# Performance work log

Measured on AMD Instinct MI355X. Metric: run time of the kernel, lower is better.

## Reference

```python
import jax, jax.numpy as jnp
import numpy as np

N_TOKENS = 32768
D_MODEL = 1024
NUM_CODES = 4096
CODE_DEPTH = 256


def setup_inputs() -> dict:
    key = jax.random.key(0)
    kx, kc, kw, kb = jax.random.split(key, 4)
    x = jax.random.normal(kx, (N_TOKENS, D_MODEL), dtype=jnp.float32)
    # codebook init mirrors the torch module: randn, row-normalized, first column zeroed
    cb = jax.random.normal(kc, (NUM_CODES, CODE_DEPTH), dtype=jnp.float32)
    cb = cb / jnp.linalg.norm(cb, axis=-1, keepdims=True)
    cb = cb.at[:, 0].set(0.0)
    W_down = jax.random.normal(kw, (D_MODEL, CODE_DEPTH), dtype=jnp.float32) * (D_MODEL ** -0.5)
    b_down = jax.random.normal(kb, (CODE_DEPTH,), dtype=jnp.float32) * 0.01
    return {"x": x, "codebook": cb, "W_down": W_down, "b_down": b_down}


def reference(x, codebook, W_down, b_down):
    # downsample d_model -> code_depth, then L2-normalize (eps=1e-6)
    z = x @ W_down + b_down                                   # [N, D]
    z = z / (jnp.linalg.norm(z, axis=-1, keepdims=True) + 1e-6)
    # squared euclidean distances to codebook[1:] (argmin of sq == argmin of cdist)
    cb = codebook[1:]                                         # [K-1, D]
    sq = (jnp.sum(z * z, axis=-1, keepdims=True)
          - 2.0 * (z @ cb.T)
          + jnp.sum(cb * cb, axis=-1))                        # [N, K-1]
    code_indices = jnp.argmin(sq, axis=-1) + 1                # [N], in [1, K)
    hard_codes = codebook[code_indices]                       # [N, D] gather
    return z, code_indices, hard_codes
```

## Files before the change

kernel.cpp:

```cpp
#include <hip/hip_runtime.h>
#include <math.h>
#include <stdint.h>

#define NT 32768
#define DM 1024
#define NC 4096
#define CD 256

#define X_F4 (DM/4)
#define W_F4 (CD/4)
#define Z_F4 (CD/4)
#define C_F4 (CD/4)

typedef __attribute__((ext_vector_type(8))) short bf16x8;
typedef __attribute__((ext_vector_type(4))) float floatx4;

__device__ __forceinline__ unsigned short f2bf(float f) {
    union { float f; uint32_t u; } v; v.f = f;
    uint32_t u = v.u;
    u += 0x7FFFu + ((u >> 16) & 1u);
    return (unsigned short)(u >> 16);
}

__device__ __forceinline__ void split8(const float4 f0, const float4 f1,
                                       bf16x8& h, bf16x8& l) {
    float f[8] = {f0.x, f0.y, f0.z, f0.w, f1.x, f1.y, f1.z, f1.w};
    #pragma unroll
    for (int j = 0; j < 8; ++j) {
        union { float f; uint32_t u; } v; v.f = f[j];
        h[j] = (short)(v.u >> 16);
        union { uint32_t u; float f; } t; t.u = v.u & 0xFFFF0000u;
        l[j] = (short)f2bf(f[j] - t.f);
    }
}

__global__ __launch_bounds__(256) void k0_prep(const float4* __restrict__ cb,
                                               float* __restrict__ hn2,
                                               ushort* __restrict__ cbb) {
    int wid = threadIdx.x >> 6, lane = threadIdx.x & 63;
    int code = blockIdx.x * 4 + wid;
    float4 c = cb[(size_t)code * C_F4 + lane];
    ushort4 h;
    h.x = f2bf(c.x); h.y = f2bf(c.y); h.z = f2bf(c.z); h.w = f2bf(c.w);
    ((ushort4*)cbb)[(size_t)code * 64 + lane] = h;
    float ss = c.x*c.x + c.y*c.y + c.z*c.z + c.w*c.w;
    #pragma unroll
    for (int m = 32; m >= 1; m >>= 1) ss += __shfl_xor(ss, m, 64);
    if (lane == 0) hn2[code] = 0.5f * ss - 2.0f;
}

__global__ __launch_bounds__(256) void k0b_wsplit(const float4* __restrict__ W,
                                                  ushort* __restrict__ WTh,
                                                  ushort* __restrict__ WTl) {
    __shared__ float lds[16][260];
    int slab = blockIdx.x;
    int tid = threadIdx.x;
    #pragma unroll
    for (int jj = 0; jj < 4; ++jj) {
        int v = jj * 256 + tid;
        int row = v >> 6, f4 = v & 63;
        float4 d = W[(size_t)(slab * 16 + row) * W_F4 + f4];
        *(float4*)&lds[row][f4 * 4] = d;
    }
    __syncthreads();
    int c = tid;
    #pragma unroll
    for (int kb = 0; kb < 2; ++kb) {
        bf16x8 h, l;
        #pragma unroll
        for (int j = 0; j < 8; ++j) {
            float x = lds[kb * 8 + j][c];
            union { float f; uint32_t u; } v; v.f = x;
            h[j] = (short)(v.u >> 16);
            union { uint32_t u; float f; } t; t.u = v.u & 0xFFFF0000u;
            l[j] = (short)f2bf(x - t.f);
        }
        size_t off = (size_t)c * 1024 + slab * 16 + kb * 8;
        *(bf16x8*)(WTh + off) = h;
        *(bf16x8*)(WTl + off) = l;
    }
}

__global__ __launch_bounds__(256, 2) void k1_gemm1(const float4* __restrict__ X,
                                                   const ushort* __restrict__ WTh,
                                                   const ushort* __restrict__ WTl,
                                                   float4* __restrict__ Zp) {
    __shared__ __align__(16) char lds[65536];
    char* Ah = lds;
    char* Al = lds + 16384;
    char* Bh = lds + 32768;
    char* Bl = lds + 49152;

    int tid  = threadIdx.x;
    int w    = tid >> 6, lane = tid & 63;
    int wm   = w >> 1, wn = w & 1;
    int c    = lane & 15, q = lane >> 4;
    int mb   = blockIdx.x >> 1, nb = blockIdx.x & 1;
    int m0   = mb * 128;
    int n0   = nb * 128;

    auto issue_loads = [&](int kt, float4* ga, bf16x8* gbh, bf16x8* gbl) {
        #pragma unroll
        for (int jj = 0; jj < 4; ++jj) {
            int v = jj * 256 + tid;
            int row = v >> 3, ch = v & 7;
            const float4* p = X + (size_t)(m0 + row) * X_F4 + kt * 16 + ch * 2;
            ga[jj * 2]     = p[0];
            ga[jj * 2 + 1] = p[1];
        }
        #pragma unroll
        for (int jj = 0; jj < 4; ++jj) {
            int v = jj * 256 + tid;
            int col = v >> 3, ch = v & 7;
            size_t off = (size_t)(n0 + col) * 1024 + kt * 64 + ch * 8;
            gbh[jj] = *(const bf16x8*)(WTh + off);
            gbl[jj] = *(const bf16x8*)(WTl + off);
        }
    };
    auto write_lds = [&](const float4* ga, const bf16x8* gbh, const bf16x8* gbl) {
        #pragma unroll
        for (int jj = 0; jj < 4; ++jj) {
            int v = jj * 256 + tid;
            int row = v >> 3, ch = v & 7;
            bf16x8 h, l;
            split8(ga[jj * 2], ga[jj * 2 + 1], h, l);
            int off = row * 128 + ((ch ^ (row & 7)) << 4);
            *(bf16x8*)(Ah + off) = h;
            *(bf16x8*)(Al + off) = l;
        }
        #pragma unroll
        for (int jj = 0; jj < 4; ++jj) {
            int v = jj * 256 + tid;
            int col = v >> 3, ch = v & 7;
            int off = col * 128 + ((ch ^ (col & 7)) << 4);
            *(bf16x8*)(Bh + off) = gbh[jj];
            *(bf16x8*)(Bl + off) = gbl[jj];
        }
    };

    floatx4 acc[4][4];
    #pragma unroll
    for (int i = 0; i < 4; ++i)
        #pragma unroll
        for (int j = 0; j < 4; ++j) acc[i][j] = (floatx4){0.f, 0.f, 0.f, 0.f};

    float4 ga[8]; bf16x8 gbh[4], gbl[4];
    issue_loads(0, ga, gbh, gbl);
    write_lds(ga, gbh, gbl);

    for (int kt = 0; kt < 16; ++kt) {
        __syncthreads();
        if (kt < 15) issue_loads(kt + 1, ga, gbh, gbl);

        #pragma unroll
        for (int ks = 0; ks < 2; ++ks) {
            bf16x8 xh[4], xl[4], wh[4], wl[4];
            #pragma unroll
            for (int i = 0; i < 4; ++i) {
                int xrow = wm * 64 + i * 16 + c;
                int xoff = xrow * 128 + (((ks * 4 + q) ^ (xrow & 7)) << 4);
                xh[i] = *(const bf16x8*)(Ah + xoff);
                xl[i] = *(const bf16x8*)(Al + xoff);
                int wrow = wn * 64 + i * 16 + c;
                int woff = wrow * 128 + (((ks * 4 + q) ^ (wrow & 7)) << 4);
                wh[i] = *(const bf16x8*)(Bh + woff);
                wl[i] = *(const bf16x8*)(Bl + woff);
            }
            #pragma unroll
            for (int xi = 0; xi < 4; ++xi)
                #pragma unroll
                for (int ni = 0; ni < 4; ++ni) {
                    acc[xi][ni] = __builtin_amdgcn_mfma_f32_16x16x32_bf16(wh[ni], xh[xi], acc[xi][ni], 0, 0, 0);
                    acc[xi][ni] = __builtin_amdgcn_mfma_f32_16x16x32_bf16(wh[ni], xl[xi], acc[xi][ni], 0, 0, 0);
                    acc[xi][ni] = __builtin_amdgcn_mfma_f32_16x16x32_bf16(wl[ni], xh[xi], acc[xi][ni], 0, 0, 0);
                }
        }

        __syncthreads();
        if (kt < 15) write_lds(ga, gbh, gbl);
    }

    #pragma unroll
    for (int xi = 0; xi < 4; ++xi) {
        int tok = m0 + wm * 64 + xi * 16 + c;
        #pragma unroll
        for (int ni = 0; ni < 4; ++ni) {
            int nf4 = nb * 32 + wn * 16 + ni * 4 + q;
            float4 o;
            o.x = acc[xi][ni][0]; o.y = acc[xi][ni][1];
            o.z = acc[xi][ni][2]; o.w = acc[xi][ni][3];
            Zp[(size_t)tok * Z_F4 + nf4] = o;
        }
    }
}

__global__ __launch_bounds__(256) void k1b_norm(float4* __restrict__ Z,
                                                const float4* __restrict__ bias) {
    int wid = threadIdx.x >> 6, lane = threadIdx.x & 63;
    int t = blockIdx.x * 4 + wid;
    float4 b = bias[lane];
    float4 z = Z[(size_t)t * Z_F4 + lane];
    z.x += b.x; z.y += b.y; z.z += b.z; z.w += b.w;
    double ss = (double)z.x*z.x + (double)z.y*z.y + (double)z.z*z.z + (double)z.w*z.w;
    #pragma unroll
    for (int m = 32; m >= 1; m >>= 1) ss += __shfl_xor(ss, m, 64);
    float inv = 1.0f / ((float)sqrt(ss) + 1e-6f);
    z.x *= inv; z.y *= inv; z.z *= inv; z.w *= inv;
    Z[(size_t)t * Z_F4 + lane] = z;
}

__global__ __launch_bounds__(256, 2) void k2_mfma(const float* __restrict__ Z,
                                                  const ushort* __restrict__ Cbb,
                                                  const float* __restrict__ hn2g,
                                                  int4* __restrict__ cands) {
    __shared__ __align__(16) char lds[32768 + 256];

    int tid  = threadIdx.x;
    int w    = tid >> 6;
    int lane = tid & 63;
    int c    = lane & 15, q = lane >> 4;
    int t0   = blockIdx.x * 64;

    bf16x8 A[4][8];
    #pragma unroll
    for (int mi = 0; mi < 4; ++mi) {
        #pragma unroll
        for (int ks = 0; ks < 8; ++ks) {
            const float* zp = Z + (size_t)(t0 + mi * 16 + c) * CD + ks * 32 + q * 8;
            float4 f0 = *(const float4*)zp;
            float4 f1 = *(const float4*)(zp + 4);
            bf16x8 a;
            a[0] = (short)f2bf(f0.x); a[1] = (short)f2bf(f0.y);
            a[2] = (short)f2bf(f0.z); a[3] = (short)f2bf(f0.w);
            a[4] = (short)f2bf(f1.x); a[5] = (short)f2bf(f1.y);
            a[6] = (short)f2bf(f1.z); a[7] = (short)f2bf(f1.w);
            A[mi][ks] = a;
        }
    }

    int baddr[8];
    #pragma unroll
    for (int ks = 0; ks < 8; ++ks)
        baddr[ks] = (w * 16 + c) * 512 + ((((ks * 4 + q) ^ c)) << 4);
    int hnaddr = 32768 + (w * 16 + c) * 4;

    auto issue_loads = [&](int ct, bf16x8* g, float& hnr) {
        #pragma unroll
        for (int jj = 0; jj < 8; ++jj) {
            int v = jj * 256 + tid;
            int row = v >> 5, ch = v & 31;
            int grow = ct * 64 + row; if (grow < 1) grow = 1;
            g[jj] = *(const bf16x8*)(Cbb + (size_t)grow * CD + ch * 8);
        }
        if (tid < 64) {
            int gc = ct * 64 + tid; if (gc < 1) gc = 1;
            hnr = hn2g[gc];
        }
    };
    auto write_lds = [&](const bf16x8* g, float hnr) {
        #pragma unroll
        for (int jj = 0; jj < 8; ++jj) {
            int v = jj * 256 + tid;
            int row = v >> 5, ch = v & 31;
            *(bf16x8*)(lds + row * 512 + ((ch ^ (row & 15)) << 4)) = g[jj];
        }
        if (tid < 64) *(float*)(lds + 32768 + tid * 4) = hnr;
    };

    uint32_t K1[16], K2[16];
    #pragma unroll
    for (int i = 0; i < 16; ++i) { K1[i] = 0u; K2[i] = 0u; }

    bf16x8 g[8]; float hnr = 0.0f;
    issue_loads(0, g, hnr);
    write_lds(g, hnr);

    for (int ct = 0; ct < 64; ++ct) {
        __syncthreads();
        bf16x8 g2[8]; float hnr2 = 0.0f;
        if (ct < 63) issue_loads(ct + 1, g2, hnr2);

        floatx4 C[4];
        #pragma unroll
        for (int mi = 0; mi < 4; ++mi) C[mi] = (floatx4){0.f, 0.f, 0.f, 0.f};

        #pragma unroll
        for (int ks = 0; ks < 8; ++ks) {
            bf16x8 Bf = *(const bf16x8*)(lds + baddr[ks]);
            #pragma unroll
            for (int mi = 0; mi < 4; ++mi)
                C[mi] = __builtin_amdgcn_mfma_f32_16x16x32_bf16(A[mi][ks], Bf, C[mi], 0, 0, 0);
        }

        float hv = *(const float*)(lds + hnaddr);
        #pragma unroll
        for (int mi = 0; mi < 4; ++mi) {
            #pragma unroll
            for (int r = 0; r < 4; ++r) {
                float sp = C[mi][r] - hv;
                union { float f; uint32_t u; } uv; uv.f = sp;
                uint32_t key = (uv.u & 0xFFFFFFC0u) | (uint32_t)ct;
                int i = mi * 4 + r;
                uint32_t lo = key < K1[i] ? key : K1[i];
                K1[i] = key > K1[i] ? key : K1[i];
                K2[i] = lo > K2[i] ? lo : K2[i];
            }
        }

        __syncthreads();
        if (ct < 63) write_lds(g2, hnr2);
    }

    __syncthreads();
    uint32_t* M = (uint32_t*)lds;
    #pragma unroll
    for (int mi = 0; mi < 4; ++mi) {
        #pragma unroll
        for (int r = 0; r < 4; ++r) {
            int tok = mi * 16 + q * 4 + r;
            int base = ((tok * 4 + w) * 16 + c) * 2;
            M[base]     = K1[mi * 4 + r];
            M[base + 1] = K2[mi * 4 + r];
        }
    }
    __syncthreads();
    if (tid < 64) {
        int tok = tid;
        uint32_t bk0 = 0, bk1 = 0, bk2 = 0, bk3 = 0;
        int      bp0 = 0, bp1 = 0, bp2 = 0, bp3 = 0;
        for (int e = 0; e < 128; ++e) {
            uint32_t key = M[tok * 128 + e];
            int pos = e >> 1;
            if (key > bk0) {
                bk3 = bk2; bp3 = bp2; bk2 = bk1; bp2 = bp1;
                bk1 = bk0; bp1 = bp0; bk0 = key; bp0 = pos;
            } else if (key > bk1) {
                bk3 = bk2; bp3 = bp2; bk2 = bk1; bp2 = bp1; bk1 = key; bp1 = pos;
            } else if (key > bk2) {
                bk3 = bk2; bp3 = bp2; bk2 = key; bp2 = pos;
            } else if (key > bk3) {
                bk3 = key; bp3 = pos;
            }
        }
        int4 out;
        out.x = (int)(bk0 & 63u) * 64 + bp0;
        out.y = (int)(bk1 & 63u) * 64 + bp1;
        out.z = (int)(bk2 & 63u) * 64 + bp2;
        out.w = (int)(bk3 & 63u) * 64 + bp3;
        cands[t0 + tok] = out;
    }
}

__global__ __launch_bounds__(256) void k3_refine(const float4* __restrict__ Z,
                                                 const float4* __restrict__ Cb,
                                                 const int4* __restrict__ cands,
                                                 float* __restrict__ idxOut,
                                                 float4* __restrict__ hardOut) {
    int wid = threadIdx.x >> 6, lane = threadIdx.x & 63;
    int t = blockIdx.x * 4 + wid;
    int4 cd = cands[t];
    int cc[4] = {cd.x, cd.y, cd.z, cd.w};
    float4 z = Z[(size_t)t * Z_F4 + lane];
    double best = -1.0e300;
    int bi = NC;
    #pragma unroll
    for (int e = 0; e < 4; ++e) {
        int idx = cc[e];
        float4 cf = Cb[(size_t)idx * C_F4 + lane];
        double dot = (double)z.x*cf.x + (double)z.y*cf.y + (double)z.z*cf.z + (double)z.w*cf.w;
        double nrm = (double)cf.x*cf.x + (double)cf.y*cf.y + (double)cf.z*cf.z + (double)cf.w*cf.w;
        #pragma unroll
        for (int m = 32; m >= 1; m >>= 1) {
            dot += __shfl_xor(dot, m, 64);
            nrm += __shfl_xor(nrm, m, 64);
        }
        double s = dot - 0.5 * nrm;
        if (idx >= 1 && (s > best || (s == best && idx < bi))) { best = s; bi = idx; }
    }
    if (lane == 0) idxOut[t] = (float)bi;
    hardOut[(size_t)t * C_F4 + lane] = Cb[(size_t)bi * C_F4 + lane];
}

extern "C" void kernel_launch(void* const* d_in, const int* in_sizes, int n_in,
                              void* d_out, int out_size, void* d_ws, size_t ws_size,
                              hipStream_t stream) {
    const float* x  = (const float*)d_in[0];
    const float* cb = (const float*)d_in[1];
    const float* w  = (const float*)d_in[2];
    const float* bd = (const float*)d_in[3];

    float* zOut    = (float*)d_out;
    float* idxOut  = zOut + (size_t)NT * CD;
    float* hardOut = idxOut + NT;

    float*  hn2   = (float*)d_ws;
    int4*   cands = (int4*)((char*)d_ws + 16384);
    ushort* cbb   = (ushort*)((char*)d_ws + 16384 + 524288);
    ushort* wth   = (ushort*)((char*)d_ws + 2637824);
    ushort* wtl   = (ushort*)((char*)d_ws + 3162112);

    k0_prep<<<NC / 4, 256, 0, stream>>>((const float4*)cb, hn2, cbb);
    k0b_wsplit<<<DM / 16, 256, 0, stream>>>((const float4*)w, wth, wtl);
    k1_gemm1<<<(NT / 128) * 2, 256, 0, stream>>>((const float4*)x, wth, wtl,
                                                 (float4*)zOut);
    k1b_norm<<<NT / 4, 256, 0, stream>>>((float4*)zOut, (const float4*)bd);
    k2_mfma<<<NT / 64, 256, 0, stream>>>(zOut, cbb, hn2, cands);
    k3_refine<<<NT / 4, 256, 0, stream>>>((const float4*)zOut, (const float4*)cb,
                                          cands, idxOut, (float4*)hardOut);
}
```

Measured before the change: 456.2 us.

## Load codebook B fragments directly from global into registers, skip LDS staging

The distance kernel no longer stages codebook tiles through shared memory with barriers. Each lane now loads its bf16 B fragments straight from global memory into registers, double-buffered across two tiles. The accumulator is pre-initialised with the negative half-norm, and the final top-4 candidate merge is split across all four waves with a padded second-stage merge. This removes per-tile __syncthreads and LDS traffic, at the cost of uncoalesced global loads (16 bytes per lane at a 512-byte stride) and more register pressure.

Result: faster. 443.3 us (-2.8%).

```diff
diff --git a/kernel.cpp b/kernel.cpp
--- a/kernel.cpp
+++ b/kernel.cpp
@@ -213,7 +213,8 @@
                                                   const ushort* __restrict__ Cbb,
                                                   const float* __restrict__ hn2g,
                                                   int4* __restrict__ cands) {
-    __shared__ __align__(16) char lds[32768 + 256];
+    __shared__ uint32_t Mld[64 * 129];
+    __shared__ uint32_t M2[64 * 34];
 
     int tid  = threadIdx.x;
     int w    = tid >> 6;
@@ -238,99 +239,92 @@
         }
     }
 
-    int baddr[8];
+    int slot = w * 16 + c;
+    const char* bbase = (const char*)Cbb + (size_t)slot * 512 + q * 16;
+    const char* b0p   = (slot == 0) ? (const char*)Cbb + 512 + q * 16 : bbase;
+    const float* hbase = hn2g + slot;
+
+    uint32_t K1[16], K2[16];
+    #pragma unroll
+    for (int i = 0; i < 16; ++i) { K1[i] = 0u; K2[i] = 0u; }
+
+    bf16x8 B0[8], B1[8];
+    float hv0, hv1;
+
     #pragma unroll
     for (int ks = 0; ks < 8; ++ks)
-        baddr[ks] = (w * 16 + c) * 512 + ((((ks * 4 + q) ^ c)) << 4);
-    int hnaddr = 32768 + (w * 16 + c) * 4;
-
-    auto issue_loads = [&](int ct, bf16x8* g, float& hnr) {
-        #pragma unroll
-        for (int jj = 0; jj < 8; ++jj) {
-            int v = jj * 256 + tid;
-            int row = v >> 5, ch = v & 31;
-            int grow = ct * 64 + row; if (grow < 1) grow = 1;
-            g[jj] = *(const bf16x8*)(Cbb + (size_t)grow * CD + ch * 8);
-        }
-        if (tid < 64) {
-            int gc = ct * 64 + tid; if (gc < 1) gc = 1;
-            hnr = hn2g[gc];
-        }
-    };
-    auto write_lds = [&](const bf16x8* g, float hnr) {
-        #pragma unroll
-        for (int jj = 0; jj < 8; ++jj) {
-            int v = jj * 256 + tid;
-            int row = v >> 5, ch = v & 31;
-            *(bf16x8*)(lds + row * 512 + ((ch ^ (row & 15)) << 4)) = g[jj];
-        }
-        if (tid < 64) *(float*)(lds + 32768 + tid * 4) = hnr;
-    };
-
-    uint32_t K1[16], K2[16];
-    #pragma unroll
-    for (int i = 0; i < 16; ++i) { K1[i] = 0u; K2[i] = 0u; }
-
-    bf16x8 g[8]; float hnr = 0.0f;
-    issue_loads(0, g, hnr);
-    write_lds(g, hnr);
-
-    for (int ct = 0; ct < 64; ++ct) {
-        __syncthreads();
-        bf16x8 g2[8]; float hnr2 = 0.0f;
-        if (ct < 63) issue_loads(ct + 1, g2, hnr2);
-
-        floatx4 C[4];
-        #pragma unroll
-        for (int mi = 0; mi < 4; ++mi) C[mi] = (floatx4){0.f, 0.f, 0.f, 0.f};
-
-        #pragma unroll
-        for (int ks = 0; ks < 8; ++ks) {
-            bf16x8 Bf = *(const bf16x8*)(lds + baddr[ks]);
-            #pragma unroll
-            for (int mi = 0; mi < 4; ++mi)
-                C[mi] = __builtin_amdgcn_mfma_f32_16x16x32_bf16(A[mi][ks], Bf, C[mi], 0, 0, 0);
-        }
-
-        float hv = *(const float*)(lds + hnaddr);
-        #pragma unroll
-        for (int mi = 0; mi < 4; ++mi) {
-            #pragma unroll
-            for (int r = 0; r < 4; ++r) {
-                float sp = C[mi][r] - hv;
-                union { float f; uint32_t u; } uv; uv.f = sp;
-                uint32_t key = (uv.u & 0xFFFFFFC0u) | (uint32_t)ct;
-                int i = mi * 4 + r;
-                uint32_t lo = key < K1[i] ? key : K1[i];
-                K1[i] = key > K1[i] ? key : K1[i];
-                K2[i] = lo > K2[i] ? lo : K2[i];
-            }
-        }
-
-        __syncthreads();
-        if (ct < 63) write_lds(g2, hnr2);
-    }
-
-    __syncthreads();
-    uint32_t* M = (uint32_t*)lds;
+        B0[ks] = *(const bf16x8*)(b0p + ks * 64);
+    hv0 = (slot == 0) ? hn2g[1] : hbase[0];
+
+    const char* bptr = bbase + 32768;
+    const float* hptr = hbase + 64;
+
+    #define K2_COMPUTE(Bc, hvc, CT)                                            \
+    {                                                                          \
+        float nh = -(hvc);                                                     \
+        floatx4 Cc[4];                                                         \
+        _Pragma("unroll")                                                      \
+        for (int mi = 0; mi < 4; ++mi) Cc[mi] = (floatx4){nh, nh, nh, nh};     \
+        _Pragma("unroll")                                                      \
+        for (int ks = 0; ks < 8; ++ks) {                                       \
+            _Pragma("unroll")                                                  \
+            for (int mi = 0; mi < 4; ++mi)                                     \
+                Cc[mi] = __builtin_amdgcn_mfma_f32_16x16x32_bf16(              \
+                    A[mi][ks], Bc[ks], Cc[mi], 0, 0, 0);                       \
+        }                                                                      \
+        _Pragma("unroll")                                                      \
+        for (int mi = 0; mi < 4; ++mi) {                                       \
+            _Pragma("unroll")                                                  \
+            for (int r = 0; r < 4; ++r) {                                      \
+                union { float f; uint32_t u; } uv; uv.f = Cc[mi][r];           \
+                uint32_t key = (uv.u & 0xFFFFFFC0u) | (uint32_t)(CT);          \
+                int i = mi * 4 + r;                                            \
+                uint32_t lo = key < K1[i] ? key : K1[i];                       \
+                K1[i] = key > K1[i] ? key : K1[i];                             \
+                K2[i] = lo > K2[i] ? lo : K2[i];                               \
+            }                                                                  \
+        }                                                                      \
+    }
+
+    for (int ct = 0; ct < 64; ct += 2) {
+        #pragma unroll
+        for (int ks = 0; ks < 8; ++ks)
+            B1[ks] = *(const bf16x8*)(bptr + ks * 64);
+        hv1 = *hptr;
+        bptr += 32768; hptr += 64;
+
+        K2_COMPUTE(B0, hv0, ct)
+
+        #pragma unroll
+        for (int ks = 0; ks < 8; ++ks)
+            B0[ks] = *(const bf16x8*)(bptr + ks * 64);
+        hv0 = *hptr;
+        bptr += 32768; hptr += 64;
+
+        K2_COMPUTE(B1, hv1, ct + 1)
+    }
+    #undef K2_COMPUTE
+
     #pragma unroll
     for (int mi = 0; mi < 4; ++mi) {
         #pragma unroll
         for (int r = 0; r < 4; ++r) {
             int tok = mi * 16 + q * 4 + r;
-            int base = ((tok * 4 + w) * 16 + c) * 2;
-            M[base]     = K1[mi * 4 + r];
-            M[base + 1] = K2[mi * 4 + r];
+            uint32_t* p = &Mld[tok * 129 + slot * 2];
+            p[0] = K1[mi * 4 + r];
+            p[1] = K2[mi * 4 + r];
         }
     }
     __syncthreads();
-    if (tid < 64) {
-        int tok = tid;
+
+    {
+        int tok = tid & 63, seg = tid >> 6;
+        const uint32_t* row = &Mld[tok * 129 + seg * 32];
         uint32_t bk0 = 0, bk1 = 0, bk2 = 0, bk3 = 0;
-        int      bp0 = 0, bp1 = 0, bp2 = 0, bp3 = 0;
-        for (int e = 0; e < 128; ++e) {
-            uint32_t key = M[tok * 128 + e];
-            int pos = e >> 1;
+        uint32_t bp0 = 0, bp1 = 0, bp2 = 0, bp3 = 0;
+        for (int e = 0; e < 32; ++e) {
+            uint32_t key = row[e];
+            uint32_t pos = (uint32_t)(seg * 16 + (e >> 1));
             if (key > bk0) {
                 bk3 = bk2; bp3 = bp2; bk2 = bk1; bp2 = bp1;
                 bk1 = bk0; bp1 = bp0; bk0 = key; bp0 = pos;
@@ -342,11 +336,39 @@
                 bk3 = key; bp3 = pos;
             }
         }
+        uint32_t* o = &M2[tok * 34 + seg * 8];
+        o[0] = bk0; o[1] = bp0; o[2] = bk1; o[3] = bp1;
+        o[4] = bk2; o[5] = bp2; o[6] = bk3; o[7] = bp3;
+    }
+    __syncthreads();
+
+    if (tid < 64) {
+        int tok = tid;
+        uint32_t bk0 = 0, bk1 = 0, bk2 = 0, bk3 = 0;
+        uint32_t bp0 = 0, bp1 = 0, bp2 = 0, bp3 = 0;
+        #pragma unroll
+        for (int h = 0; h < 4; ++h) {
+            #pragma unroll
+            for (int j = 0; j < 4; ++j) {
+                uint32_t key = M2[tok * 34 + h * 8 + j * 2];
+                uint32_t pos = M2[tok * 34 + h * 8 + j * 2 + 1];
+                if (key > bk0) {
+                    bk3 = bk2; bp3 = bp2; bk2 = bk1; bp2 = bp1;
+                    bk1 = bk0; bp1 = bp0; bk0 = key; bp0 = pos;
+                } else if (key > bk1) {
+                    bk3 = bk2; bp3 = bp2; bk2 = bk1; bp2 = bp1; bk1 = key; bp1 = pos;
+                } else if (key > bk2) {
+                    bk3 = bk2; bp3 = bp2; bk2 = key; bp2 = pos;
+                } else if (key > bk3) {
+                    bk3 = key; bp3 = pos;
+                }
+            }
+        }
         int4 out;
-        out.x = (int)(bk0 & 63u) * 64 + bp0;
-        out.y = (int)(bk1 & 63u) * 64 + bp1;
-        out.z = (int)(bk2 & 63u) * 64 + bp2;
-        out.w = (int)(bk3 & 63u) * 64 + bp3;
+        out.x = (int)(bk0 & 63u) * 64 + (int)bp0;
+        out.y = (int)(bk1 & 63u) * 64 + (int)bp1;
+        out.z = (int)(bk2 & 63u) * 64 + (int)bp2;
+        out.w = (int)(bk3 & 63u) * 64 + (int)bp3;
         cands[t0 + tok] = out;
     }
 }
```

## Fold codebook norm into padded K column and stream codebook directly into registers

Applied to the files above, without the earlier changes.

The codebook is stored in bf16 with 16 extra padded columns that hold a hi/lo split of the norm bias. This turns the bias subtraction into one more 32x32x16 MFMA step against a constant column in the token operand. The distance kernel drops its LDS staging and barriers per tile. Each wave holds 32 tokens in registers and streams codebook rows straight from global memory (L2), double-buffering them in registers. It keeps a top-4 per lane instead of a top-2 and launches with 1 block per CU and 128 tokens per block. The trade is much higher register pressure and lower occupancy, and codebook reads no longer go through LDS sharing, in exchange for fewer syncs and better MFMA shape efficiency.

New measurement: 441.0 us. -3.3%, faster.

```diff
diff --git a/kernel.cpp b/kernel.cpp
--- a/kernel.cpp
+++ b/kernel.cpp
@@ -12,8 +12,13 @@
 #define Z_F4 (CD/4)
 #define C_F4 (CD/4)
 
+#define CDE 272
+#define CDE_B (CDE*2)
+#define TILE_B (32*CDE_B)
+
 typedef __attribute__((ext_vector_type(8))) short bf16x8;
 typedef __attribute__((ext_vector_type(4))) float floatx4;
+typedef __attribute__((ext_vector_type(16))) float floatx16;
 
 __device__ __forceinline__ unsigned short f2bf(float f) {
     union { float f; uint32_t u; } v; v.f = f;
@@ -35,18 +40,27 @@
 }
 
 __global__ __launch_bounds__(256) void k0_prep(const float4* __restrict__ cb,
-                                               float* __restrict__ hn2,
-                                               ushort* __restrict__ cbb) {
+                                               ushort* __restrict__ cbb2) {
     int wid = threadIdx.x >> 6, lane = threadIdx.x & 63;
     int code = blockIdx.x * 4 + wid;
     float4 c = cb[(size_t)code * C_F4 + lane];
     ushort4 h;
     h.x = f2bf(c.x); h.y = f2bf(c.y); h.z = f2bf(c.z); h.w = f2bf(c.w);
-    ((ushort4*)cbb)[(size_t)code * 64 + lane] = h;
+    *(ushort4*)(cbb2 + (size_t)code * CDE + lane * 4) = h;
     float ss = c.x*c.x + c.y*c.y + c.z*c.z + c.w*c.w;
     #pragma unroll
     for (int m = 32; m >= 1; m >>= 1) ss += __shfl_xor(ss, m, 64);
-    if (lane == 0) hn2[code] = 0.5f * ss - 2.0f;
+    if (lane == 0) {
+        float nh = 2.0f - 0.5f * ss;
+        union { float f; uint32_t u; } v; v.f = nh;
+        uint32_t uh = v.u & 0xFFFF0000u;
+        union { uint32_t u; float f; } t; t.u = uh;
+        ushort* p = cbb2 + (size_t)code * CDE + 256;
+        p[0] = (ushort)(uh >> 16);
+        p[1] = f2bf(nh - t.f);
+        #pragma unroll
+        for (int i = 2; i < 16; ++i) p[i] = 0;
+    }
 }
 
 __global__ __launch_bounds__(256) void k0b_wsplit(const float4* __restrict__ W,
@@ -209,145 +223,115 @@
     Z[(size_t)t * Z_F4 + lane] = z;
 }
 
-__global__ __launch_bounds__(256, 2) void k2_mfma(const float* __restrict__ Z,
-                                                  const ushort* __restrict__ Cbb,
-                                                  const float* __restrict__ hn2g,
+__global__ __launch_bounds__(256, 1) void k2_mfma(const float* __restrict__ Z,
+                                                  const ushort* __restrict__ Cbb2,
                                                   int4* __restrict__ cands) {
-    __shared__ __align__(16) char lds[32768 + 256];
+    __shared__ uint32_t Mk[128][2][4];
 
     int tid  = threadIdx.x;
-    int w    = tid >> 6;
+    int wm   = tid >> 6;
     int lane = tid & 63;
-    int c    = lane & 15, q = lane >> 4;
-    int t0   = blockIdx.x * 64;
-
-    bf16x8 A[4][8];
-    #pragma unroll
-    for (int mi = 0; mi < 4; ++mi) {
-        #pragma unroll
-        for (int ks = 0; ks < 8; ++ks) {
-            const float* zp = Z + (size_t)(t0 + mi * 16 + c) * CD + ks * 32 + q * 8;
-            float4 f0 = *(const float4*)zp;
-            float4 f1 = *(const float4*)(zp + 4);
-            bf16x8 a;
-            a[0] = (short)f2bf(f0.x); a[1] = (short)f2bf(f0.y);
-            a[2] = (short)f2bf(f0.z); a[3] = (short)f2bf(f0.w);
-            a[4] = (short)f2bf(f1.x); a[5] = (short)f2bf(f1.y);
-            a[6] = (short)f2bf(f1.z); a[7] = (short)f2bf(f1.w);
-            A[mi][ks] = a;
-        }
-    }
-
-    int baddr[8];
-    #pragma unroll
-    for (int ks = 0; ks < 8; ++ks)
-        baddr[ks] = (w * 16 + c) * 512 + ((((ks * 4 + q) ^ c)) << 4);
-    int hnaddr = 32768 + (w * 16 + c) * 4;
-
-    auto issue_loads = [&](int ct, bf16x8* g, float& hnr) {
-        #pragma unroll
-        for (int jj = 0; jj < 8; ++jj) {
-            int v = jj * 256 + tid;
-            int row = v >> 5, ch = v & 31;
-            int grow = ct * 64 + row; if (grow < 1) grow = 1;
-            g[jj] = *(const bf16x8*)(Cbb + (size_t)grow * CD + ch * 8);
-        }
-        if (tid < 64) {
-            int gc = ct * 64 + tid; if (gc < 1) gc = 1;
-            hnr = hn2g[gc];
+    int r    = lane & 31;
+    int hi   = lane >> 5;
+    int t0   = blockIdx.x * 128;
+
+    bf16x8 Bt[17];
+    #pragma unroll
+    for (int f = 0; f < 16; ++f) {
+        const float* zp = Z + (size_t)(t0 + wm * 32 + r) * CD + f * 16 + hi * 8;
+        float4 f0 = *(const float4*)zp;
+        float4 f1 = *(const float4*)(zp + 4);
+        bf16x8 b;
+        b[0] = (short)f2bf(f0.x); b[1] = (short)f2bf(f0.y);
+        b[2] = (short)f2bf(f0.z); b[3] = (short)f2bf(f0.w);
+        b[4] = (short)f2bf(f1.x); b[5] = (short)f2bf(f1.y);
+        b[6] = (short)f2bf(f1.z); b[7] = (short)f2bf(f1.w);
+        Bt[f] = b;
+    }
+    {
+        bf16x8 b = (bf16x8){0, 0, 0, 0, 0, 0, 0, 0};
+        if (hi == 0) { b[0] = (short)0x3F80; b[1] = (short)0x3F80; }
+        Bt[16] = b;
+    }
+
+    int r0 = (r == 0) ? 1 : r;
+    const char* abase   = (const char*)Cbb2;
+    const char* ap_lane = abase + r * CDE_B + hi * 16;
+    const char* ap0     = abase + r0 * CDE_B + hi * 16;
+
+    uint32_t K1v = 0, K2v = 0, K3v = 0, K4v = 0;
+
+    bf16x8 A0[17], A1[17];
+    #pragma unroll
+    for (int f = 0; f < 17; ++f) A0[f] = *(const bf16x8*)(ap0 + f * 32);
+
+    const char* ap = ap_lane + TILE_B;
+
+    auto compute = [&](const bf16x8 (&Ax)[17], int ct) {
+        floatx16 Cc;
+        #pragma unroll
+        for (int i = 0; i < 16; ++i) Cc[i] = 0.0f;
+        #pragma unroll
+        for (int f = 0; f < 17; ++f)
+            Cc = __builtin_amdgcn_mfma_f32_32x32x16_bf16(Ax[f], Bt[f], Cc, 0, 0, 0);
+        #pragma unroll
+        for (int reg = 0; reg < 16; ++reg) {
+            union { float f; uint32_t u; } uv; uv.f = Cc[reg];
+            uint32_t k = (uv.u & 0xFFFFF800u) | ((uint32_t)ct << 4) | (uint32_t)reg;
+            uint32_t t;
+            t = k < K1v ? k : K1v;  K1v = k > K1v ? k : K1v;  k = t;
+            t = k < K2v ? k : K2v;  K2v = k > K2v ? k : K2v;  k = t;
+            t = k < K3v ? k : K3v;  K3v = k > K3v ? k : K3v;  k = t;
+            K4v = k > K4v ? k : K4v;
         }
     };
-    auto write_lds = [&](const bf16x8* g, float hnr) {
-        #pragma unroll
-        for (int jj = 0; jj < 8; ++jj) {
-            int v = jj * 256 + tid;
-            int row = v >> 5, ch = v & 31;
-            *(bf16x8*)(lds + row * 512 + ((ch ^ (row & 15)) << 4)) = g[jj];
-        }
-        if (tid < 64) *(float*)(lds + 32768 + tid * 4) = hnr;
-    };
-
-    uint32_t K1[16], K2[16];
-    #pragma unroll
-    for (int i = 0; i < 16; ++i) { K1[i] = 0u; K2[i] = 0u; }
-
-    bf16x8 g[8]; float hnr = 0.0f;
-    issue_loads(0, g, hnr);
-    write_lds(g, hnr);
-
-    for (int ct = 0; ct < 64; ++ct) {
-        __syncthreads();
-        bf16x8 g2[8]; float hnr2 = 0.0f;
-        if (ct < 63) issue_loads(ct + 1, g2, hnr2);
-
-        floatx4 C[4];
-        #pragma unroll
-        for (int mi = 0; mi < 4; ++mi) C[mi] = (floatx4){0.f, 0.f, 0.f, 0.f};
-
-        #pragma unroll
-        for (int ks = 0; ks < 8; ++ks) {
-            bf16x8 Bf = *(const bf16x8*)(lds + baddr[ks]);
-            #pragma unroll
-            for (int mi = 0; mi < 4; ++mi)
-                C[mi] = __builtin_amdgcn_mfma_f32_16x16x32_bf16(A[mi][ks], Bf, C[mi], 0, 0, 0);
-        }
-
-        float hv = *(const float*)(lds + hnaddr);
-        #pragma unroll
-        for (int mi = 0; mi < 4; ++mi) {
-            #pragma unroll
-            for (int r = 0; r < 4; ++r) {
-                float sp = C[mi][r] - hv;
-                union { float f; uint32_t u; } uv; uv.f = sp;
-                uint32_t key = (uv.u & 0xFFFFFFC0u) | (uint32_t)ct;
-                int i = mi * 4 + r;
-                uint32_t lo = key < K1[i] ? key : K1[i];
-                K1[i] = key > K1[i] ? key : K1[i];
-                K2[i] = lo > K2[i] ? lo : K2[i];
+
+    for (int ct = 0; ct < 128; ct += 2) {
+        #pragma unroll
+        for (int f = 0; f < 17; ++f) A1[f] = *(const bf16x8*)(ap + f * 32);
+        ap += TILE_B;
+        compute(A0, ct);
+        const char* apn = (ct + 2 < 128) ? ap : ap_lane;
+        #pragma unroll
+        for (int f = 0; f < 17; ++f) A0[f] = *(const bf16x8*)(apn + f * 32);
+        ap += TILE_B;
+        compute(A1, ct + 1);
+        if ((ct & 15) == 14) __builtin_amdgcn_s_barrier();
+    }
+
+    int lt = wm * 32 + r;
+    Mk[lt][hi][0] = K1v; Mk[lt][hi][1] = K2v;
+    Mk[lt][hi][2] = K3v; Mk[lt][hi][3] = K4v;
+    __syncthreads();
+
+    if (tid < 128) {
+        uint32_t bk0 = 0, bk1 = 0, bk2 = 0, bk3 = 0;
+        uint32_t be0 = 0, be1 = 0, be2 = 0, be3 = 0;
+        #pragma unroll
+        for (int e = 0; e < 8; ++e) {
+            uint32_t key = Mk[tid][e >> 2][e & 3];
+            if (key > bk0) {
+                bk3 = bk2; be3 = be2; bk2 = bk1; be2 = be1;
+                bk1 = bk0; be1 = be0; bk0 = key; be0 = (uint32_t)e;
+            } else if (key > bk1) {
+                bk3 = bk2; be3 = be2; bk2 = bk1; be2 = be1; bk1 = key; be1 = (uint32_t)e;
+            } else if (key > bk2) {
+                bk3 = bk2; be3 = be2; bk2 = key; be2 = (uint32_t)e;
+            } else if (key > bk3) {
+                bk3 = key; be3 = (uint32_t)e;
             }
         }
-
-        __syncthreads();
-        if (ct < 63) write_lds(g2, hnr2);
-    }
-
-    __syncthreads();
-    uint32_t* M = (uint32_t*)lds;
-    #pragma unroll
-    for (int mi = 0; mi < 4; ++mi) {
-        #pragma unroll
-        for (int r = 0; r < 4; ++r) {
-            int tok = mi * 16 + q * 4 + r;
-            int base = ((tok * 4 + w) * 16 + c) * 2;
-            M[base]     = K1[mi * 4 + r];
-            M[base + 1] = K2[mi * 4 + r];
-        }
-    }
-    __syncthreads();
-    if (tid < 64) {
-        int tok = tid;
-        uint32_t bk0 = 0, bk1 = 0, bk2 = 0, bk3 = 0;
-        int      bp0 = 0, bp1 = 0, bp2 = 0, bp3 = 0;
-        for (int e = 0; e < 128; ++e) {
-            uint32_t key = M[tok * 128 + e];
-            int pos = e >> 1;
-            if (key > bk0) {
-                bk3 = bk2; bp3 = bp2; bk2 = bk1; bp2 = bp1;
-                bk1 = bk0; bp1 = bp0; bk0 = key; bp0 = pos;
-            } else if (key > bk1) {
-                bk3 = bk2; bp3 = bp2; bk2 = bk1; bp2 = bp1; bk1 = key; bp1 = pos;
-            } else if (key > bk2) {
-                bk3 = bk2; bp3 = bp2; bk2 = key; bp2 = pos;
-            } else if (key > bk3) {
-                bk3 = key; bp3 = pos;
-            }
-        }
+        auto dec = [&](uint32_t key, uint32_t e) -> int {
+            int ct = (int)((key >> 4) & 127u);
+            int rg = (int)(key & 15u);
+            int row = (rg & 3) + 8 * (rg >> 2) + 4 * (int)(e >> 2);
+            int code = ct * 32 + row;
+            return code < 1 ? 1 : code;
+        };
         int4 out;
-        out.x = (int)(bk0 & 63u) * 64 + bp0;
-        out.y = (int)(bk1 & 63u) * 64 + bp1;
-        out.z = (int)(bk2 & 63u) * 64 + bp2;
-        out.w = (int)(bk3 & 63u) * 64 + bp3;
-        cands[t0 + tok] = out;
+        out.x = dec(bk0, be0); out.y = dec(bk1, be1);
+        out.z = dec(bk2, be2); out.w = dec(bk3, be3);
+        cands[t0 + tid] = out;
     }
 }
 
@@ -393,18 +377,17 @@
     float* idxOut  = zOut + (size_t)NT * CD;
     float* hardOut = idxOut + NT;
 
-    float*  hn2   = (float*)d_ws;
-    int4*   cands = (int4*)((char*)d_ws + 16384);
-    ushort* cbb   = (ushort*)((char*)d_ws + 16384 + 524288);
-    ushort* wth   = (ushort*)((char*)d_ws + 2637824);
-    ushort* wtl   = (ushort*)((char*)d_ws + 3162112);
-
-    k0_prep<<<NC / 4, 256, 0, stream>>>((const float4*)cb, hn2, cbb);
+    int4*   cands = (int4*)d_ws;
+    ushort* cbb2  = (ushort*)((char*)d_ws + 524288);
+    ushort* wth   = (ushort*)((char*)d_ws + 2752512);
+    ushort* wtl   = (ushort*)((char*)d_ws + 3276800);
+
+    k0_prep<<<NC / 4, 256, 0, stream>>>((const float4*)cb, cbb2);
     k0b_wsplit<<<DM / 16, 256, 0, stream>>>((const float4*)w, wth, wtl);
     k1_gemm1<<<(NT / 128) * 2, 256, 0, stream>>>((const float4*)x, wth, wtl,
                                                  (float4*)zOut);
     k1b_norm<<<NT / 4, 256, 0, stream>>>((float4*)zOut, (const float4*)bd);
-    k2_mfma<<<NT / 64, 256, 0, stream>>>(zOut, cbb, hn2, cands);
+    k2_mfma<<<NT / 128, 256, 0, stream>>>(zOut, cbb2, cands);
     k3_refine<<<NT / 4, 256, 0, stream>>>((const float4*)zOut, (const float4*)cb,
                                           cands, idxOut, (float4*)hardOut);
 }
```
